# Kernel tuning notes

Hardware: AMD Instinct MI355X
Metric: run time of the kernel (lower is better)

The kernel has to match this reference:

```python
import jax, jax.numpy as jnp
import numpy as np


def bilinear_align_corners(p, H, W):
    # p: [B, C, h, w] -> [B, C, H, W], matches F.interpolate(mode='bilinear', align_corners=True)
    b, c, h, w = p.shape
    ys = jnp.linspace(0.0, h - 1.0, H)
    xs = jnp.linspace(0.0, w - 1.0, W)
    y0 = jnp.floor(ys).astype(jnp.int32)
    x0 = jnp.floor(xs).astype(jnp.int32)
    y1 = jnp.minimum(y0 + 1, h - 1)
    x1 = jnp.minimum(x0 + 1, w - 1)
    wy = (ys - y0.astype(p.dtype))[:, None]          # [H,1]
    wx = (xs - x0.astype(p.dtype))                   # [W]
    rows = p[:, :, y0, :] * (1 - wy) + p[:, :, y1, :] * wy   # [B,C,H,w]
    out = rows[:, :, :, x0] * (1 - wx) + rows[:, :, :, x1] * wx  # [B,C,H,W]
    return out


def conv1x1(x, W, b):
    return jnp.einsum('bchw,oc->bohw', x, W) + b[None, :, None, None]


def scan_axis(feat, A_bar, B_bar, axis):
    # selective recurrence h_i = A_i * stop_grad(h_{i-1}) + B_i * x_i along `axis`
    f = jnp.moveaxis(feat, axis, 0)
    A = jnp.moveaxis(A_bar, axis, 0)
    B = jnp.moveaxis(B_bar, axis, 0)

    def step(prev, inp):
        a_i, b_i, x_i = inp
        h = a_i * jax.lax.stop_gradient(prev) + b_i * x_i
        return h, h

    _, hs = jax.lax.scan(step, jnp.zeros_like(f[0]), (A, B, f))
    return jnp.moveaxis(hs, 0, axis)


def setup_inputs() -> dict:
    key = jax.random.key(0)
    ks = jax.random.split(key, 12)
    Bsz, Cin, H, W = 4, 64, 256, 256
    hid = 128
    s_in = 1.0 / np.sqrt(Cin)
    s_hid = 1.0 / np.sqrt(hid)
    return {
        'x': jax.random.normal(ks[0], (Bsz, Cin, H, W), jnp.float32),
        'prior': jax.random.normal(ks[1], (Bsz, 1, 64, 64), jnp.float32),
        'W_in': jax.random.uniform(ks[2], (hid, Cin), jnp.float32, -s_in, s_in),
        'b_in': jax.random.uniform(ks[3], (hid,), jnp.float32, -s_in, s_in),
        'W_out': jax.random.uniform(ks[4], (Cin, hid), jnp.float32, -s_hid, s_hid),
        'b_out': jax.random.uniform(ks[5], (Cin,), jnp.float32, -s_hid, s_hid),
        'W_delta': jax.random.uniform(ks[6], (hid, hid), jnp.float32, -s_hid, s_hid),
        'b_delta': jax.random.uniform(ks[7], (hid,), jnp.float32, -s_hid, s_hid),
        'W_B': jax.random.uniform(ks[8], (hid, hid), jnp.float32, -s_hid, s_hid),
        'b_B': jax.random.uniform(ks[9], (hid,), jnp.float32, -s_hid, s_hid),
        'A_param': jax.random.normal(ks[10], (hid,), jnp.float32),
        'lambda_delta': jnp.float32(0.1),
        'alpha': jnp.float32(0.1),
        'gamma': jnp.float32(0.1),
    }


def reference(x, prior, W_in, b_in, W_out, b_out, W_delta, b_delta, W_B, b_B,
              A_param, lambda_delta, alpha, gamma):
    Bsz, C, H, W = x.shape
    prior_up = jnp.clip(bilinear_align_corners(prior, H, W), -1.0, 1.0)
    x_proj = conv1x1(x, W_in, b_in)
    delta = jax.nn.softplus(conv1x1(x_proj, W_delta, b_delta) + lambda_delta * prior_up)
    B_k = conv1x1(x_proj, W_B, b_B) * (1.0 + alpha * prior_up)
    A = -jnp.exp(A_param)[None, :, None, None]
    A_bar = jnp.exp(delta * A)
    B_bar = delta * B_k
    # dim=0 in torch code scans along W (axis 3); dim=1 scans along H (axis 2)
    scanned = scan_axis(x_proj, A_bar, B_bar, 3) + scan_axis(x_proj, A_bar, B_bar, 2)
    out = conv1x1(scanned, W_out, b_out)
    return (x + gamma * out, prior_up)
```

## Files before the change

kernel.cpp:

```cpp
#include <hip/hip_runtime.h>
#include <hip/hip_bf16.h>

#define OUT1 16777216
#define BIG  33554432

typedef _Float16 half8 __attribute__((ext_vector_type(8)));
typedef float    floatx4 __attribute__((ext_vector_type(4)));

struct __align__(8) h4s { _Float16 x, y, z, w; };
struct __align__(16) au16 { h4s a, u; };

__global__ __launch_bounds__(256) void k_comb(const float* __restrict__ W_in, const float* __restrict__ b_in,
        const float* __restrict__ W_delta, const float* __restrict__ b_delta,
        const float* __restrict__ W_B, const float* __restrict__ b_B,
        const float* __restrict__ A_param, const float* __restrict__ W_out,
        _Float16* __restrict__ Wch, float* __restrict__ bcv, float* __restrict__ negA,
        _Float16* __restrict__ Wof, float* __restrict__ bct){
    int i = blockIdx.x*256 + threadIdx.x;
    if (i < 24576){
        int r = i >> 6, c = i & 63;
        float v;
        if (r < 128) v = W_in[i];
        else if (r < 256){
            int rr = r-128; float s = 0.f;
            for (int k=0;k<128;k++) s = fmaf(W_delta[(rr<<7)+k], W_in[(k<<6)+c], s);
            v = s;
        } else {
            int rr = r-256; float s = 0.f;
            for (int k=0;k<128;k++) s = fmaf(W_B[(rr<<7)+k], W_in[(k<<6)+c], s);
            v = s;
        }
        Wch[i] = (_Float16)v;
    } else if (i < 24960){
        int r = i - 24576; float v;
        if (r < 128) v = b_in[r];
        else if (r < 256){
            int rr=r-128; float s = b_delta[rr];
            for (int k=0;k<128;k++) s = fmaf(W_delta[(rr<<7)+k], b_in[k], s);
            v = s;
        } else {
            int rr=r-256; float s = b_B[rr];
            for (int k=0;k<128;k++) s = fmaf(W_B[(rr<<7)+k], b_in[k], s);
            v = s;
        }
        bcv[r] = v;
    } else if (i < 25088){
        negA[i-24960] = -expf(A_param[i-24960]);
    } else if (i < 33280){
        Wof[i-25088] = (_Float16)W_out[i-25088];
    } else if (i < 33792){
        int j = i - 33280;
        int c = j >> 2, comp = j & 3;
        float v;
        if (comp == 0) v = b_in[c];
        else if (comp == 1){
            float s = b_delta[c];
            for (int k=0;k<128;k++) s = fmaf(W_delta[(c<<7)+k], b_in[k], s);
            v = s;
        } else if (comp == 2){
            float s = b_B[c];
            for (int k=0;k<128;k++) s = fmaf(W_B[(c<<7)+k], b_in[k], s);
            v = s;
        } else {
            v = -expf(A_param[c]);
        }
        bct[j] = v;
    }
}

__global__ __launch_bounds__(512, 4) void k_proj_mfma(const float* __restrict__ x, const float* __restrict__ prior,
        const _Float16* __restrict__ Wch, const float* __restrict__ bct,
        const float* __restrict__ lam_p, const float* __restrict__ alp_p,
        float* __restrict__ pu, au16* __restrict__ AU){
    __shared__ _Float16 Ws[24576];

    const int t    = threadIdx.x;
    const int lane = t & 63;
    const int wave = t >> 6;
    const int col  = lane & 15;
    const int quad = lane >> 4;

    const int bl      = blockIdx.x;
    const int b       = bl >> 7;
    const int px_base = (bl & 127) << 9;

    {
        const float4* wsrc = (const float4*)Wch;
        #pragma unroll
        for (int i = 0; i < 6; i++){
            int c = t + (i << 9);
            int row = c >> 3, part = c & 7;
            float4 v = wsrc[c];
            int byteoff = ((row << 7) + (part << 4)) ^ ((row & 7) << 4);
            *(float4*)((char*)Ws + byteoff) = v;
        }
    }

    const float lamv = lam_p[0], alpv = alp_p[0];
    const float* xcol = x + ((size_t)b<<22) + col;

    float xf0[8], xf1[8];
    {
        const float* xp = xcol + px_base + (wave<<4);
        #pragma unroll
        for (int j = 0; j < 8; j++){
            xf0[j] = xp[(size_t)(quad*8 + j) << 16];
            xf1[j] = xp[(size_t)(quad*8 + j + 32) << 16];
        }
    }

    __syncthreads();

    const int qb = quad << 4;
    const char* wsb = (const char*)Ws;

    #pragma unroll 1
    for (int ch = 0; ch < 4; ch++){
        const int pxw = px_base + (ch << 7) + (wave << 4);

        half8 aX0, aX1;
        #pragma unroll
        for (int j = 0; j < 8; j++){
            aX0[j] = (_Float16)xf0[j];
            aX1[j] = (_Float16)xf1[j];
        }

        if (ch < 3){
            const float* xn = xcol + pxw + 128;
            #pragma unroll
            for (int j = 0; j < 8; j++){
                xf0[j] = xn[(size_t)(quad*8 + j) << 16];
                xf1[j] = xn[(size_t)(quad*8 + j + 32) << 16];
            }
        }

        const float scale = 63.0f/255.0f;
        int yy = pxw >> 8;
        float sy = yy*scale;
        int y0 = min((int)floorf(sy), 63);
        int y1 = min(y0+1, 63);
        float wy = sy - (float)y0;
        const float* pb0 = prior + (b<<12) + (y0<<6);
        const float* pb1 = prior + (b<<12) + (y1<<6);
        int xx0 = (pxw & 255) + (quad<<2);
        float lpu[4], apu[4];
        float4 puo;
        #pragma unroll
        for (int r = 0; r < 4; r++){
            float sx = (float)(xx0 + r)*scale;
            int x0 = min((int)floorf(sx), 63);
            int x1 = min(x0+1, 63);
            float wx = sx - (float)x0;
            float r0 = pb0[x0]*(1.f-wy) + pb1[x0]*wy;
            float r1 = pb0[x1]*(1.f-wy) + pb1[x1]*wy;
            float pv = fminf(fmaxf(r0*(1.f-wx) + r1*wx, -1.f), 1.f);
            ((float*)&puo)[r] = pv;
            lpu[r] = lamv * pv;
            apu[r] = fmaf(alpv, pv, 1.f);
        }
        *(float4*)(pu + (b<<16) + pxw + (quad<<2)) = puo;

        #pragma unroll 2
        for (int ct = 0; ct < 8; ct++){
            int rI = (ct << 4) + col;
            int xr = (rI & 7) << 4;
            half8 wI0 = *(const half8*)(wsb + ((( rI       << 7) +      qb) ^ xr));
            half8 wI1 = *(const half8*)(wsb + ((( rI       << 7) + 64 + qb) ^ xr));
            half8 wD0 = *(const half8*)(wsb + ((((rI + 128)<< 7) +      qb) ^ xr));
            half8 wD1 = *(const half8*)(wsb + ((((rI + 128)<< 7) + 64 + qb) ^ xr));
            half8 wB0 = *(const half8*)(wsb + ((((rI + 256)<< 7) +      qb) ^ xr));
            half8 wB1 = *(const half8*)(wsb + ((((rI + 256)<< 7) + 64 + qb) ^ xr));

            floatx4 aI = (floatx4){0.f,0.f,0.f,0.f};
            floatx4 aD = (floatx4){0.f,0.f,0.f,0.f};
            floatx4 aB = (floatx4){0.f,0.f,0.f,0.f};
            aI = __builtin_amdgcn_mfma_f32_16x16x32_f16(aX0, wI0, aI, 0, 0, 0);
            aD = __builtin_amdgcn_mfma_f32_16x16x32_f16(aX0, wD0, aD, 0, 0, 0);
            aB = __builtin_amdgcn_mfma_f32_16x16x32_f16(aX0, wB0, aB, 0, 0, 0);
            aI = __builtin_amdgcn_mfma_f32_16x16x32_f16(aX1, wI1, aI, 0, 0, 0);
            aD = __builtin_amdgcn_mfma_f32_16x16x32_f16(aX1, wD1, aD, 0, 0, 0);
            aB = __builtin_amdgcn_mfma_f32_16x16x32_f16(aX1, wB1, aB, 0, 0, 0);

            int c = (ct<<4) + col;
            float4 bv = *(const float4*)(bct + (c<<2));
            au16 ov;
            #pragma unroll
            for (int r = 0; r < 4; r++){
                float sI = aI[r] + bv.x;
                float sD = aD[r] + bv.y;
                float sB = aB[r] + bv.z;
                float dpre  = sD + lpu[r];
                float delta = fmaxf(dpre, 0.f) + __logf(1.f + __expf(-fabsf(dpre)));
                float ab    = __expf(bv.w * delta);
                float uu    = delta * sB * apu[r] * sI;
                (&ov.a.x)[r] = (_Float16)ab;
                (&ov.u.x)[r] = (_Float16)uu;
            }
            size_t u = (((size_t)((b<<7) + c)) << 14) + (pxw >> 2) + quad;
            AU[u] = ov;
        }
    }
}

__global__ __launch_bounds__(512) void k_scan_wh(const au16* __restrict__ AU, _Float16* __restrict__ Sh){
    __shared__ float As[8][256], Us[8][256], Wsc[8][256];
    __shared__ _Float16 Shs[8][256];

    const int t    = threadIdx.x;
    const int lane = t & 63;
    const int wave = t >> 6;
    const size_t plane = (size_t)blockIdx.x;
    const size_t bI = plane >> 7, cI = plane & 127;

    float Hcol = 0.f;

    const size_t ub = (plane << 14) + (wave << 6) + lane;

    au16 cA = AU[ub];
    au16 cB = AU[ub + 512];

    auto proc = [&](au16 cur, int gg){
        float ax=(float)cur.a.x, ay=(float)cur.a.y, az=(float)cur.a.z, aw=(float)cur.a.w;
        float ux=(float)cur.u.x, uy=(float)cur.u.y, uz=(float)cur.u.z, uw=(float)cur.u.w;

        float A = ax, U = ux;
        U = fmaf(ay, U, uy); A *= ay;
        U = fmaf(az, U, uz); A *= az;
        U = fmaf(aw, U, uw); A *= aw;
        #pragma unroll
        for (int off=1; off<64; off<<=1){
            float Apv = __shfl_up(A, off, 64);
            float Upv = __shfl_up(U, off, 64);
            if (lane >= off){ U = fmaf(A, Upv, U); A *= Apv; }
        }
        float h = __shfl_up(U, 1, 64);
        if (lane == 0) h = 0.f;
        float4 o;
        h = fmaf(ax, h, ux); o.x = h;
        h = fmaf(ay, h, uy); o.y = h;
        h = fmaf(az, h, uz); o.z = h;
        h = fmaf(aw, h, uw); o.w = h;

        int c0 = lane << 2;
        *(float4*)&As [wave][c0] = (float4){ax,ay,az,aw};
        *(float4*)&Us [wave][c0] = (float4){ux,uy,uz,uw};
        *(float4*)&Wsc[wave][c0] = o;

        asm volatile("s_waitcnt lgkmcnt(0)" ::: "memory");
        __builtin_amdgcn_sched_barrier(0);
        __builtin_amdgcn_s_barrier();
        __builtin_amdgcn_sched_barrier(0);

        if (t < 256){
            #pragma unroll
            for (int v = 0; v < 8; v++){
                Hcol = fmaf(As[v][t], Hcol, Us[v][t]);
                Shs[v][t] = (_Float16)(Hcol + Wsc[v][t]);
            }
        }

        asm volatile("s_waitcnt lgkmcnt(0)" ::: "memory");
        __builtin_amdgcn_sched_barrier(0);
        __builtin_amdgcn_s_barrier();
        __builtin_amdgcn_sched_barrier(0);

        h4s sv = *(h4s*)&Shs[wave][lane << 2];
        size_t hh = (size_t)((gg << 3) + wave);
        *(h4s*)(Sh + (bI<<23) + (hh<<15) + (cI<<8) + (lane<<2)) = sv;
    };

    #pragma unroll 1
    for (int g = 0; g < 32; g += 2){
        proc(cA, g);
        if (g + 2 < 32) cA = AU[ub + (size_t)(g + 2) * 512];
        proc(cB, g + 1);
        if (g + 3 < 32) cB = AU[ub + (size_t)(g + 3) * 512];
    }
}

__global__ __launch_bounds__(256, 4) void k_out_mfma(const float* __restrict__ x, const _Float16* __restrict__ Sh,
        const _Float16* __restrict__ Wof, const float* __restrict__ bout, const float* __restrict__ gam_p,
        float* __restrict__ out){
    const int t    = threadIdx.x;
    const int lane = t & 63;
    const int wave = t >> 6;
    const int col  = lane & 15;
    const int quad = lane >> 4;
    const int b    = blockIdx.x >> 8;
    const int hh   = blockIdx.x & 255;
    const int p0   = hh << 8;
    const int wn0  = wave << 6;

    const _Float16* shb = Sh + ((size_t)b<<23) + ((size_t)hh<<15);

    floatx4 acc[4][4];
    #pragma unroll
    for (int mt = 0; mt < 4; mt++)
        #pragma unroll
        for (int nt = 0; nt < 4; nt++)
            acc[mt][nt] = (floatx4){0.f,0.f,0.f,0.f};

    #pragma unroll
    for (int kc = 0; kc < 4; kc++){
        half8 af[4];
        #pragma unroll
        for (int mt = 0; mt < 4; mt++)
            #pragma unroll
            for (int j = 0; j < 8; j++)
                af[mt][j] = shb[((kc*32 + quad*8 + j)<<8) + wn0 + mt*16 + col];
        half8 bf[4];
        #pragma unroll
        for (int nt = 0; nt < 4; nt++)
            bf[nt] = *(const half8*)(Wof + (nt*16 + col)*128 + kc*32 + quad*8);
        #pragma unroll
        for (int mt = 0; mt < 4; mt++)
            #pragma unroll
            for (int nt = 0; nt < 4; nt++)
                acc[mt][nt] = __builtin_amdgcn_mfma_f32_16x16x32_f16(af[mt], bf[nt], acc[mt][nt], 0, 0, 0);
    }

    const float gv = gam_p[0];
    #pragma unroll
    for (int nt = 0; nt < 4; nt++){
        int o = nt*16 + col;
        float bo = bout[o];
        #pragma unroll
        for (int mt = 0; mt < 4; mt++){
            size_t idx = (((size_t)(b*64 + o))<<16) + p0 + wn0 + mt*16 + (quad<<2);
            float4 xv = *(const float4*)(x + idx);
            float4 ov;
            ov.x = fmaf(gv, acc[mt][nt][0] + bo, xv.x);
            ov.y = fmaf(gv, acc[mt][nt][1] + bo, xv.y);
            ov.z = fmaf(gv, acc[mt][nt][2] + bo, xv.z);
            ov.w = fmaf(gv, acc[mt][nt][3] + bo, xv.w);
            *(float4*)(out + idx) = ov;
        }
    }
}

extern "C" void kernel_launch(void* const* d_in, const int* in_sizes, int n_in,
                              void* d_out, int out_size, void* d_ws, size_t ws_size,
                              hipStream_t stream){
    const float* x       = (const float*)d_in[0];
    const float* prior   = (const float*)d_in[1];
    const float* W_in    = (const float*)d_in[2];
    const float* b_in    = (const float*)d_in[3];
    const float* W_out   = (const float*)d_in[4];
    const float* b_out   = (const float*)d_in[5];
    const float* W_delta = (const float*)d_in[6];
    const float* b_delta = (const float*)d_in[7];
    const float* W_B     = (const float*)d_in[8];
    const float* b_B     = (const float*)d_in[9];
    const float* A_param = (const float*)d_in[10];
    const float* lam     = (const float*)d_in[11];
    const float* alp     = (const float*)d_in[12];
    const float* gam     = (const float*)d_in[13];

    float* out = (float*)d_out;
    float* pu  = out + OUT1;

    float* ws        = (float*)d_ws;
    _Float16* Wch    = (_Float16*)ws;
    float* bcv       = ws + 12288;
    float* negA      = ws + 12672;
    _Float16* Wof    = (_Float16*)(ws + 12800);
    float* bct       = ws + 16896;
    au16* AU         = (au16*)(ws + 32768);
    _Float16* Sh     = (_Float16*)(AU + BIG/4);

    hipLaunchKernelGGL(k_comb,   dim3(132),   dim3(256), 0, stream, W_in, b_in, W_delta, b_delta,
                       W_B, b_B, A_param, W_out, Wch, bcv, negA, Wof, bct);
    hipLaunchKernelGGL(k_proj_mfma, dim3(512), dim3(512), 0, stream,
                       x, prior, Wch, bct, lam, alp, pu, AU);
    hipLaunchKernelGGL(k_scan_wh, dim3(512), dim3(512), 0, stream, AU, Sh);
    hipLaunchKernelGGL(k_out_mfma, dim3(1024), dim3(256), 0, stream, x, Sh, Wof, b_out, gam, out);
}
```

Before: 273.6 us.

## Widen scan blocks to 16 waves and store A/U tiles in half precision LDS

The H/W scan kernel now runs 1024 threads per plane, so 16 rows are processed per group and there are 16 groups per plane instead of 32. This halves the number of block barriers and serial column-phase steps per plane. The column phase now walks 16 rows per step, so its serial chain per step is longer. A and U are kept in LDS as fp16 rather than fp32, and the double-buffered prefetch becomes a single-register prefetch. The risks are lower occupancy per block and less load latency hiding, since only one load is in flight per wave.

```diff
diff --git a/kernel.cpp b/kernel.cpp
--- a/kernel.cpp
+++ b/kernel.cpp
@@ -202,9 +202,10 @@
     }
 }
 
-__global__ __launch_bounds__(512) void k_scan_wh(const au16* __restrict__ AU, _Float16* __restrict__ Sh){
-    __shared__ float As[8][256], Us[8][256], Wsc[8][256];
-    __shared__ _Float16 Shs[8][256];
+__global__ __launch_bounds__(1024) void k_scan_wh(const au16* __restrict__ AU, _Float16* __restrict__ Sh){
+    __shared__ _Float16 As2[16][256], Us2[16][256];
+    __shared__ float    Wsc[16][256];
+    __shared__ _Float16 Shs[16][256];
 
     const int t    = threadIdx.x;
     const int lane = t & 63;
@@ -214,37 +215,42 @@
 
     float Hcol = 0.f;
 
-    const size_t ub = (plane << 14) + (wave << 6) + lane;
-
-    au16 cA = AU[ub];
-    au16 cB = AU[ub + 512];
-
-    auto proc = [&](au16 cur, int gg){
-        float ax=(float)cur.a.x, ay=(float)cur.a.y, az=(float)cur.a.z, aw=(float)cur.a.w;
-        float ux=(float)cur.u.x, uy=(float)cur.u.y, uz=(float)cur.u.z, uw=(float)cur.u.w;
-
-        float A = ax, U = ux;
-        U = fmaf(ay, U, uy); A *= ay;
-        U = fmaf(az, U, uz); A *= az;
-        U = fmaf(aw, U, uw); A *= aw;
-        #pragma unroll
-        for (int off=1; off<64; off<<=1){
-            float Apv = __shfl_up(A, off, 64);
-            float Upv = __shfl_up(U, off, 64);
-            if (lane >= off){ U = fmaf(A, Upv, U); A *= Apv; }
-        }
-        float h = __shfl_up(U, 1, 64);
-        if (lane == 0) h = 0.f;
-        float4 o;
-        h = fmaf(ax, h, ux); o.x = h;
-        h = fmaf(ay, h, uy); o.y = h;
-        h = fmaf(az, h, uz); o.z = h;
-        h = fmaf(aw, h, uw); o.w = h;
-
-        int c0 = lane << 2;
-        *(float4*)&As [wave][c0] = (float4){ax,ay,az,aw};
-        *(float4*)&Us [wave][c0] = (float4){ux,uy,uz,uw};
-        *(float4*)&Wsc[wave][c0] = o;
+    const size_t ub = (plane << 14) + lane;
+
+    au16 cur = AU[ub + ((size_t)wave << 6)];
+
+    #pragma unroll 1
+    for (int g = 0; g < 16; g++){
+        au16 nxt = cur;
+        if (g < 15) nxt = AU[ub + ((size_t)(((g + 1) << 4) + wave) << 6)];
+
+        {
+            float ax=(float)cur.a.x, ay=(float)cur.a.y, az=(float)cur.a.z, aw=(float)cur.a.w;
+            float ux=(float)cur.u.x, uy=(float)cur.u.y, uz=(float)cur.u.z, uw=(float)cur.u.w;
+
+            float A = ax, U = ux;
+            U = fmaf(ay, U, uy); A *= ay;
+            U = fmaf(az, U, uz); A *= az;
+            U = fmaf(aw, U, uw); A *= aw;
+            #pragma unroll
+            for (int off=1; off<64; off<<=1){
+                float Apv = __shfl_up(A, off, 64);
+                float Upv = __shfl_up(U, off, 64);
+                if (lane >= off){ U = fmaf(A, Upv, U); A *= Apv; }
+            }
+            float h = __shfl_up(U, 1, 64);
+            if (lane == 0) h = 0.f;
+            float4 o;
+            h = fmaf(ax, h, ux); o.x = h;
+            h = fmaf(ay, h, uy); o.y = h;
+            h = fmaf(az, h, uz); o.z = h;
+            h = fmaf(aw, h, uw); o.w = h;
+
+            int c0 = lane << 2;
+            *(h4s*)&As2[wave][c0] = cur.a;
+            *(h4s*)&Us2[wave][c0] = cur.u;
+            *(float4*)&Wsc[wave][c0] = o;
+        }
 
         asm volatile("s_waitcnt lgkmcnt(0)" ::: "memory");
         __builtin_amdgcn_sched_barrier(0);
@@ -253,8 +259,8 @@
 
         if (t < 256){
             #pragma unroll
-            for (int v = 0; v < 8; v++){
-                Hcol = fmaf(As[v][t], Hcol, Us[v][t]);
+            for (int v = 0; v < 16; v++){
+                Hcol = fmaf((float)As2[v][t], Hcol, (float)Us2[v][t]);
                 Shs[v][t] = (_Float16)(Hcol + Wsc[v][t]);
             }
         }
@@ -264,17 +270,13 @@
         __builtin_amdgcn_s_barrier();
         __builtin_amdgcn_sched_barrier(0);
 
-        h4s sv = *(h4s*)&Shs[wave][lane << 2];
-        size_t hh = (size_t)((gg << 3) + wave);
-        *(h4s*)(Sh + (bI<<23) + (hh<<15) + (cI<<8) + (lane<<2)) = sv;
-    };
-
-    #pragma unroll 1
-    for (int g = 0; g < 32; g += 2){
-        proc(cA, g);
-        if (g + 2 < 32) cA = AU[ub + (size_t)(g + 2) * 512];
-        proc(cB, g + 1);
-        if (g + 3 < 32) cB = AU[ub + (size_t)(g + 3) * 512];
+        {
+            h4s sv = *(h4s*)&Shs[wave][lane << 2];
+            size_t hh = (size_t)((g << 4) + wave);
+            *(h4s*)(Sh + (bI<<23) + (hh<<15) + (cI<<8) + (lane<<2)) = sv;
+        }
+
+        cur = nxt;
     }
 }
 
@@ -372,6 +374,6 @@
                        W_B, b_B, A_param, W_out, Wch, bcv, negA, Wof, bct);
     hipLaunchKernelGGL(k_proj_mfma, dim3(512), dim3(512), 0, stream,
                        x, prior, Wch, bct, lam, alp, pu, AU);
-    hipLaunchKernelGGL(k_scan_wh, dim3(512), dim3(512), 0, stream, AU, Sh);
+    hipLaunchKernelGGL(k_scan_wh, dim3(512), dim3(1024), 0, stream, AU, Sh);
     hipLaunchKernelGGL(k_out_mfma, dim3(1024), dim3(256), 0, stream, x, Sh, Wof, b_out, gam, out);
 }
```

Result: no change. 270.3 us (median of 2 runs) (-1.2%).
